# Kernel optimization log

Hardware: AMD Instinct MI355X
Metric: run time of the kernel (lower is better)

The kernel has to match this reference:

```python
import jax, jax.numpy as jnp
import numpy as np

EPS = 1e-6
NEG = -100000.0


def _ln(x):
    # LayerNorm, elementwise_affine=False, eps=1e-6
    mu = jnp.mean(x, axis=-1, keepdims=True)
    var = jnp.mean((x - mu) ** 2, axis=-1, keepdims=True)
    return (x - mu) * jax.lax.rsqrt(var + EPS)


def _split_heads(x, h):
    b, s, d = x.shape
    return x.reshape(b, s, h, d // h).transpose(0, 2, 1, 3)  # [B,H,S,Dh]


def _merge_heads(x):
    b, h, s, dh = x.shape
    return x.transpose(0, 2, 1, 3).reshape(b, s, h * dh)


def _conv_pool(x, w):
    # grouped Conv2d(num_heads -> num_heads, kernel=(4,1), stride=(4,1), groups=num_heads, bias=False)
    # x: [B,H,S,Dh] as NCHW, w: [H,1,4,1] as OIHW
    return jax.lax.conv_general_dilated(
        x, w, window_strides=(4, 1), padding='VALID',
        dimension_numbers=('NCHW', 'OIHW', 'NCHW'),
        feature_group_count=x.shape[1])


def setup_inputs() -> dict:
    key = jax.random.key(0)
    ks = jax.random.split(key, 14)
    B, S, M, D, QKV, MLP, H = 4, 4096, 256, 768, 768, 3072, 12
    std = 0.02
    f = lambda k, shp: jax.random.normal(k, shp, jnp.float32) * std
    return {
        'x': jax.random.normal(ks[0], (B, S, D), jnp.float32),
        'memory': jax.random.normal(ks[1], (B, M, D), jnp.float32),
        'mask': jax.random.randint(ks[2], (B, S), 0, 2).astype(jnp.int32),
        'Wq': f(ks[3], (QKV, D)), 'Wk': f(ks[4], (QKV, D)),
        'Wv': f(ks[5], (QKV, D)), 'Wo': f(ks[6], (D, QKV)),
        'conv_w': f(ks[7], (H, 1, 4, 1)),
        'Uq': f(ks[8], (QKV, D)), 'Uk': f(ks[9], (QKV, D)),
        'Uv': f(ks[10], (QKV, D)), 'Uo': f(ks[11], (D, QKV)),
        'W1': f(ks[12], (MLP, D)), 'W2': f(ks[13], (D, MLP)),
    }


def reference(x, memory, mask, Wq, Wk, Wv, Wo, conv_w, Uq, Uk, Uv, Uo, W1, W2):
    H = conv_w.shape[0]
    maskf = mask.astype(x.dtype)                       # [B,S]

    # ---- pack: ConvAttention(memory as q, x as k/v); conv downsamples k/v ->
    #      shape_change=True so the k_mask is skipped (as in the torch code).
    q = _split_heads(memory @ Wq.T, H)                 # [B,H,M,Dh], unit temperature (log_temp=0)
    k = _split_heads(x @ Wk.T, H)                      # [B,H,S,Dh]
    v = _split_heads(x @ Wv.T, H)
    k = _conv_pool(k, conv_w)                          # [B,H,S//4,Dh]
    v = _conv_pool(v, conv_w)
    logits = jnp.einsum('bhqd,bhkd->bhqk', q, k)
    att = jax.nn.softmax(logits, axis=-1)
    packed = _merge_heads(att @ v) @ Wo.T              # [B,M,D]

    # ---- unpack: TAttention(x as q, packed as k/v) with q_mask injection
    head_dim = Uq.shape[0] // H
    uq = _split_heads(x @ Uq.T, H) * (1.0 / jnp.sqrt(jnp.asarray(head_dim, x.dtype)))
    uk = _split_heads(packed @ Uk.T, H)                # [B,H,M,Dh]
    uv = _split_heads(packed @ Uv.T, H)
    ulogits = jnp.einsum('bhqd,bhkd->bhqk', uq, uk)    # [B,H,S,M]
    ulogits = ulogits + NEG * (1.0 - maskf[:, None, :, None])
    uatt = jax.nn.softmax(ulogits, axis=-1)
    unpacked = _merge_heads(uatt @ uv) @ Uo.T          # [B,S,D]

    unpacked = unpacked * maskf[..., None]
    q_out = _ln(x + unpacked)
    m_out = _ln(memory + packed)

    # FFN: Linear -> GELU(exact) -> Linear (dropout=0)
    h = jax.nn.gelu(jnp.einsum('bsd,md->bsm', q_out, W1), approximate=False)
    y = jnp.einsum('bsm,dm->bsd', h, W2)
    y = y * maskf[..., None]
    q_out = _ln(q_out + y)
    return (q_out, m_out)
```

## Files before the change

kernel.cpp:

```cpp
#include <hip/hip_runtime.h>
#include <hip/hip_bf16.h>
#include <math.h>


typedef unsigned short u16;
typedef __attribute__((ext_vector_type(8))) short bf8v;
typedef __attribute__((ext_vector_type(4))) float f4v;
typedef __attribute__((ext_vector_type(4))) unsigned short us4v;

#define AS1 __attribute__((address_space(1)))
#define AS3 __attribute__((address_space(3)))

__device__ __forceinline__ void gld_lds16(const void* g, void* l) {
  __builtin_amdgcn_global_load_lds((const AS1 unsigned int*)g,
                                   (AS3 unsigned int*)l, 16, 0, 0);
}

__device__ __forceinline__ u16 bf16_rne(float x) {
  unsigned u = __float_as_uint(x);
  return (u16)((u + 0x7fffu + ((u >> 16) & 1u)) >> 16);
}
__device__ __forceinline__ float bf16_to_f(u16 h) {
  return __uint_as_float(((unsigned)h) << 16);
}

struct Cvt8 {
  const float* src[8];
  u16* dst[8];
  int n4[8];
  float sc[8];
  int cum[9];
  int ns;
};
__global__ __launch_bounds__(256) void tobf16_multi_kernel(Cvt8 c) {
  int b = blockIdx.x;
  int seg = 0;
  while (seg + 1 < c.ns && b >= c.cum[seg + 1]) ++seg;
  int i = (b - c.cum[seg]) * 256 + threadIdx.x;
  if (i >= c.n4[seg]) return;
  const float sc = c.sc[seg];
  float4 v = ((const float4*)c.src[seg])[i];
  us4v h;
  h[0] = bf16_rne(v.x * sc); h[1] = bf16_rne(v.y * sc);
  h[2] = bf16_rne(v.z * sc); h[3] = bf16_rne(v.w * sc);
  ((us4v*)c.dst[seg])[i] = h;
}

template <int BM, int BN, int GELU, int OMODE>
__global__ __launch_bounds__(BM * 2) void bgemm_kernel(
    const u16* __restrict__ A, const u16* __restrict__ B,
    float* __restrict__ Cf, u16* __restrict__ Cb, int M, int N, int K,
    int lda, int ldb, int ldc, long long aSB, long long aSH, long long bSB,
    long long bSH, long long cSB, long long cSH, int HB, float scale) {
  constexpr int NJ = BN / 32;
  constexpr int NW = BM / 32;
  constexpr int LPB = (BN / 16) / NW;
  constexpr int VW = 2 + LPB;
  __shared__ u16 smA[3][BM * 32];
  __shared__ u16 smB[3][BN * 32];
  const int t = threadIdx.x;
  const int w = t >> 6, lane = t & 63;
  const int z = blockIdx.z;
  const int bb = z / HB, hh = z % HB;
  const u16* Ab = A + bb * aSB + hh * aSH;
  const u16* Bb = B + bb * bSB + hh * bSH;
  float* Cfb = (OMODE != 1) ? (Cf + bb * cSB + hh * cSH) : nullptr;
  u16* Cbb = (OMODE >= 1) ? (Cb + bb * cSB + hh * cSH) : nullptr;

  const int gx = gridDim.x;
  const int nwg = gx * gridDim.y;
  int f = blockIdx.x + gx * blockIdx.y;
  if ((nwg & 7) == 0) {
    const int cpx = nwg >> 3;
    f = (f & 7) * cpx + (f >> 3);
  }
  const int row0 = (f / gx) * BM, col0 = (f % gx) * BN;

  const int brow_l = lane >> 2;
  const int bchunk = ((lane & 3) ^ ((lane >> 3) & 3)) * 8;
  const int fr = lane & 15;
  const int fq = lane >> 4;
  const int fco = (fq ^ ((lane >> 1) & 3)) * 8;
  const int wr = (w >> 1) * 64, wc = (w & 1) * (BN / 2);

  f4v acc[4][NJ];
#pragma unroll
  for (int i = 0; i < 4; ++i)
#pragma unroll
    for (int j = 0; j < NJ; ++j) acc[i][j] = {0.f, 0.f, 0.f, 0.f};

  const int NT = K >> 5;

  auto stage = [&](int tile, int buf) {
    const int k0 = tile << 5;
#pragma unroll
    for (int i = 0; i < 2; ++i) {
      const int g = w * 2 + i;
      const int r = g * 16 + brow_l;
      gld_lds16(Ab + (long long)(row0 + r) * lda + k0 + bchunk,
                &smA[buf][g * 512 + lane * 8]);
    }
#pragma unroll
    for (int i = 0; i < LPB; ++i) {
      const int g = w * LPB + i;
      const int r = g * 16 + brow_l;
      gld_lds16(Bb + (long long)(col0 + r) * ldb + k0 + bchunk,
                &smB[buf][g * 512 + lane * 8]);
    }
  };
#define WAIT_L()                                            \
  do {                                                      \
    if constexpr (VW == 4)                                  \
      asm volatile("s_waitcnt vmcnt(4)" ::: "memory");      \
    else                                                    \
      asm volatile("s_waitcnt vmcnt(3)" ::: "memory");      \
  } while (0)

  stage(0, 0);
  if (NT > 1) {
    stage(1, 1);
    WAIT_L();
  } else {
    asm volatile("s_waitcnt vmcnt(0)" ::: "memory");
  }
  __builtin_amdgcn_sched_barrier(0);
  __builtin_amdgcn_s_barrier();

  int cur = 0;
  for (int tt = 0; tt < NT; ++tt) {
    const int nn2 = (cur + 2 >= 3) ? cur - 1 : cur + 2;
    if (tt + 2 < NT) stage(tt + 2, nn2);
    {
      bf8v af[4], bfr[NJ];
#pragma unroll
      for (int mi = 0; mi < 4; ++mi)
        af[mi] = *(const bf8v*)&smA[cur][(wr + mi * 16 + fr) * 32 + fco];
#pragma unroll
      for (int nj = 0; nj < NJ; ++nj)
        bfr[nj] = *(const bf8v*)&smB[cur][(wc + nj * 16 + fr) * 32 + fco];
      __builtin_amdgcn_s_setprio(1);
#pragma unroll
      for (int mi = 0; mi < 4; ++mi)
#pragma unroll
        for (int nj = 0; nj < NJ; ++nj)
          acc[mi][nj] = __builtin_amdgcn_mfma_f32_16x16x32_bf16(
              af[mi], bfr[nj], acc[mi][nj], 0, 0, 0);
      __builtin_amdgcn_s_setprio(0);
    }
    if (tt + 2 < NT) {
      WAIT_L();
    } else if (tt + 1 < NT) {
      asm volatile("s_waitcnt vmcnt(0)" ::: "memory");
    }
    __builtin_amdgcn_sched_barrier(0);
    __builtin_amdgcn_s_barrier();
    cur = (cur + 1 >= 3) ? 0 : cur + 1;
  }
#undef WAIT_L

#pragma unroll
  for (int mi = 0; mi < 4; ++mi)
#pragma unroll
    for (int nj = 0; nj < NJ; ++nj) {
      const int col = col0 + wc + nj * 16 + fr;
      const long long base =
          (long long)(row0 + wr + mi * 16 + fq * 4) * ldc + col;
#pragma unroll
      for (int j = 0; j < 4; ++j) {
        float v = acc[mi][nj][j] * scale;
        if (GELU) v = 0.5f * v * (1.f + erff(v * 0.70710678118654752f));
        const long long idx = base + (long long)j * ldc;
        if (OMODE != 1) Cfb[idx] = v;
        if (OMODE >= 1) Cbb[idx] = bf16_rne(v);
      }
    }
}

__global__ __launch_bounds__(512) void fused_pack_attn(
    const u16* __restrict__ q, const u16* __restrict__ k,
    const u16* __restrict__ vt, u16* __restrict__ o) {
  __shared__ char pool[110080];
  u16* smQ = (u16*)pool;
  u16* smK = (u16*)(pool + 16384);
  u16* Pbuf = (u16*)(pool + 32768);
  u16* smV = (u16*)(pool + 98304);
  float* partial = (float*)(pool + 106496);
  float* mold = (float*)(pool + 108544);
  float* fbuf = (float*)(pool + 109056);
  float* srow = (float*)(pool + 109568);

  const int t = threadIdx.x;
  const int w = t >> 6, lane = t & 63;
  const int z = blockIdx.z;
  const int b = z / 12, h = z % 12;
  const int qrow0 = b * 256 + blockIdx.x * 128;
  const long long kvbase = ((long long)(b * 12 + h)) * 65536;

  const int fr = lane & 15, fq = lane >> 4;
  const int fco = (fq ^ ((lane >> 1) & 3)) * 8;
  const int brow_l = lane >> 2;
  const int bchunk = ((lane & 3) ^ ((lane >> 3) & 3)) * 8;
  const int wr = (w >> 2) * 64, wc = (w & 3) * 64;
  const int wrp = (w >> 1) * 32, wcp = (w & 1) * 32;

#pragma unroll
  for (int i = 0; i < 2; ++i) {
    const int g = w * 2 + i;
    const int plane = g >> 3, grp = g & 7;
    gld_lds16(q + (long long)(qrow0 + grp * 16 + brow_l) * 768 + h * 64 +
                  plane * 32 + bchunk,
              smQ + plane * 4096 + grp * 512 + lane * 8);
  }
  if (t < 128) {
    mold[t] = -3.0e38f;
    srow[t] = 0.f;
  }

  f4v acc2[2][2];
#pragma unroll
  for (int i = 0; i < 2; ++i)
#pragma unroll
    for (int j = 0; j < 2; ++j) acc2[i][j] = {0.f, 0.f, 0.f, 0.f};

  for (int kc = 0; kc < 4; ++kc) {
    f4v acc[4][4];
#pragma unroll
    for (int i = 0; i < 4; ++i)
#pragma unroll
      for (int j = 0; j < 4; ++j) acc[i][j] = {0.f, 0.f, 0.f, 0.f};

#pragma unroll
    for (int khalf = 0; khalf < 2; ++khalf) {
      __syncthreads();
#pragma unroll
      for (int i = 0; i < 2; ++i) {
        const int g = w * 2 + i;
        gld_lds16(k + kvbase +
                      (long long)(kc * 256 + g * 16 + brow_l) * 64 +
                      khalf * 32 + bchunk,
                  smK + g * 512 + lane * 8);
      }
      __syncthreads();
#pragma unroll
      for (int mi = 0; mi < 4; ++mi) {
        const bf8v a0 =
            *(const bf8v*)&smQ[khalf * 4096 + (wr + mi * 16 + fr) * 32 + fco];
#pragma unroll
        for (int nj = 0; nj < 4; ++nj) {
          const bf8v b0 = *(const bf8v*)&smK[(wc + nj * 16 + fr) * 32 + fco];
          acc[mi][nj] =
              __builtin_amdgcn_mfma_f32_16x16x32_bf16(a0, b0, acc[mi][nj], 0, 0, 0);
        }
      }
    }
    __syncthreads();

#pragma unroll
    for (int mi = 0; mi < 4; ++mi)
#pragma unroll
      for (int j = 0; j < 4; ++j) {
        float m = fmaxf(fmaxf(acc[mi][0][j], acc[mi][1][j]),
                        fmaxf(acc[mi][2][j], acc[mi][3][j]));
#pragma unroll
        for (int o2 = 1; o2 < 16; o2 <<= 1) m = fmaxf(m, __shfl_xor(m, o2));
        if (fr == 0) partial[(w & 3) * 128 + wr + mi * 16 + fq * 4 + j] = m;
      }
    __syncthreads();
    if (t < 128) {
      const float cm = fmaxf(fmaxf(partial[t], partial[128 + t]),
                             fmaxf(partial[256 + t], partial[384 + t]));
      const float mnew = fmaxf(mold[t], cm);
      fbuf[t] = exp2f(mold[t] - mnew);
      mold[t] = mnew;
    }
    __syncthreads();

#pragma unroll
    for (int mi = 0; mi < 4; ++mi)
#pragma unroll
      for (int j = 0; j < 4; ++j) {
        const int row = wr + mi * 16 + fq * 4 + j;
        const float rm = mold[row];
        float s = 0.f;
#pragma unroll
        for (int nj = 0; nj < 4; ++nj) {
          const float e = exp2f(acc[mi][nj][j] - rm);
          s += e;
          const int col = wc + nj * 16 + fr;
          const int kc2 = col >> 5, kloc = col & 31;
          Pbuf[kc2 * 4096 + row * 32 + (((kloc >> 3) ^ ((row >> 1) & 3)) * 8) +
               (kloc & 7)] = bf16_rne(e);
        }
#pragma unroll
        for (int o2 = 1; o2 < 16; o2 <<= 1) s += __shfl_xor(s, o2);
        if (fr == 0) partial[(w & 3) * 128 + row] = s;
      }
    if (w < 4) {
      gld_lds16(vt + kvbase + (long long)(w * 16 + brow_l) * 1024 + kc * 256 +
                    bchunk,
                smV + w * 512 + lane * 8);
    }
    __syncthreads();
    if (t < 128)
      srow[t] = srow[t] * fbuf[t] +
                ((partial[t] + partial[128 + t]) +
                 (partial[256 + t] + partial[384 + t]));
    __syncthreads();

#pragma unroll
    for (int mi = 0; mi < 2; ++mi)
#pragma unroll
      for (int j = 0; j < 4; ++j) {
        const float fr_ = fbuf[wrp + mi * 16 + fq * 4 + j];
        acc2[mi][0][j] *= fr_;
        acc2[mi][1][j] *= fr_;
      }

    for (int sk = 0; sk < 8; ++sk) {
      const int cur = (sk & 1) * 2048;
      if (sk < 7 && w < 4) {
        gld_lds16(vt + kvbase + (long long)(w * 16 + brow_l) * 1024 +
                      kc * 256 + (sk + 1) * 32 + bchunk,
                  smV + (2048 - cur) + w * 512 + lane * 8);
      }
#pragma unroll
      for (int mi = 0; mi < 2; ++mi) {
        const bf8v pa =
            *(const bf8v*)&Pbuf[sk * 4096 + (wrp + mi * 16 + fr) * 32 + fco];
#pragma unroll
        for (int nj = 0; nj < 2; ++nj) {
          const bf8v v0 =
              *(const bf8v*)&smV[cur + (wcp + nj * 16 + fr) * 32 + fco];
          acc2[mi][nj] =
              __builtin_amdgcn_mfma_f32_16x16x32_bf16(pa, v0, acc2[mi][nj], 0, 0, 0);
        }
      }
      __syncthreads();
    }
  }

  if (t < 128) fbuf[t] = 1.f / srow[t];
  __syncthreads();
  const long long ooff = (long long)qrow0 * 768 + h * 64;
#pragma unroll
  for (int mi = 0; mi < 2; ++mi)
#pragma unroll
    for (int nj = 0; nj < 2; ++nj)
#pragma unroll
      for (int j = 0; j < 4; ++j) {
        const int row = wrp + mi * 16 + fq * 4 + j;
        const int col = wcp + nj * 16 + fr;
        o[ooff + (long long)row * 768 + col] =
            bf16_rne(acc2[mi][nj][j] * fbuf[row]);
      }
}

__global__ __launch_bounds__(512) void fused_unpack_attn(
    const u16* __restrict__ q, int ldq, const u16* __restrict__ k, int ldk,
    const u16* __restrict__ vt, u16* __restrict__ o) {
  __shared__ char pool[76800];
  u16* smA = (u16*)pool;
  u16* smB = (u16*)(pool + 8192);
  u16* Pbuf = (u16*)pool;
  u16* smV = (u16*)(pool + 65536);
  float* partial = (float*)(pool + 73728);
  float* rowmax = (float*)(pool + 75776);
  float* rowsum = (float*)(pool + 76288);

  const int t = threadIdx.x;
  const int w = t >> 6, lane = t & 63;
  const int z = blockIdx.z;
  const int b = z / 12, h = z % 12;
  const int q0 = blockIdx.x * 128;

  const long long qoff = (long long)(b * 4096 + q0) * ldq + h * 64;
  const long long koff = (long long)(b * 256) * ldk + h * 64;
  const long long vbase = ((long long)(b * 12 + h)) * 16384;
  const long long ooff = (long long)(b * 4096 + q0) * 768 + h * 64;

  const int fr = lane & 15, fq = lane >> 4;
  const int fco = (fq ^ ((lane >> 1) & 3)) * 8;
  const int brow_l = lane >> 2;
  const int bchunk = ((lane & 3) ^ ((lane >> 3) & 3)) * 8;

  const int wr = (w >> 2) * 64, wc = (w & 3) * 64;
  f4v acc[4][4];
#pragma unroll
  for (int i = 0; i < 4; ++i)
#pragma unroll
    for (int j = 0; j < 4; ++j) acc[i][j] = {0.f, 0.f, 0.f, 0.f};

  for (int k0 = 0; k0 < 64; k0 += 32) {
    __syncthreads();
#pragma unroll
    for (int i = 0; i < 2; ++i) {
      const int g = w * 2 + i;
      const int r = g * 16 + brow_l;
      gld_lds16(k + koff + (long long)r * ldk + k0 + bchunk,
                smB + g * 512 + lane * 8);
    }
    {
      const int r = w * 16 + brow_l;
      gld_lds16(q + qoff + (long long)r * ldq + k0 + bchunk,
                smA + w * 512 + lane * 8);
    }
    __syncthreads();
#pragma unroll
    for (int mi = 0; mi < 4; ++mi) {
      const bf8v a0 = *(const bf8v*)&smA[(wr + mi * 16 + fr) * 32 + fco];
#pragma unroll
      for (int nj = 0; nj < 4; ++nj) {
        const bf8v b0 = *(const bf8v*)&smB[(wc + nj * 16 + fr) * 32 + fco];
        acc[mi][nj] = __builtin_amdgcn_mfma_f32_16x16x32_bf16(a0, b0, acc[mi][nj], 0, 0, 0);
      }
    }
  }
  __syncthreads();

  if (w < 4) {
    const int r = w * 16 + brow_l;
    gld_lds16(vt + vbase + (long long)r * 256 + bchunk,
              smV + w * 512 + lane * 8);
  }

#pragma unroll
  for (int mi = 0; mi < 4; ++mi)
#pragma unroll
    for (int j = 0; j < 4; ++j) {
      float m = fmaxf(fmaxf(acc[mi][0][j], acc[mi][1][j]),
                      fmaxf(acc[mi][2][j], acc[mi][3][j]));
#pragma unroll
      for (int o2 = 1; o2 < 16; o2 <<= 1) m = fmaxf(m, __shfl_xor(m, o2));
      if (fr == 0) partial[(w & 3) * 128 + wr + mi * 16 + fq * 4 + j] = m;
    }
  __syncthreads();
  if (t < 128)
    rowmax[t] = fmaxf(fmaxf(partial[t], partial[128 + t]),
                      fmaxf(partial[256 + t], partial[384 + t]));
  __syncthreads();
#pragma unroll
  for (int mi = 0; mi < 4; ++mi)
#pragma unroll
    for (int j = 0; j < 4; ++j) {
      const int row = wr + mi * 16 + fq * 4 + j;
      const float rm = rowmax[row];
      float s = 0.f;
#pragma unroll
      for (int nj = 0; nj < 4; ++nj) {
        const float e = exp2f(acc[mi][nj][j] - rm);
        s += e;
        const int col = wc + nj * 16 + fr;
        const int kc = col >> 5, kloc = col & 31;
        Pbuf[kc * 4096 + row * 32 + (((kloc >> 3) ^ ((row >> 1) & 3)) * 8) +
             (kloc & 7)] = bf16_rne(e);
      }
#pragma unroll
      for (int o2 = 1; o2 < 16; o2 <<= 1) s += __shfl_xor(s, o2);
      if (fr == 0) partial[(w & 3) * 128 + row] = s;
    }
  __syncthreads();
  if (t < 128)
    rowsum[t] = 1.f / ((partial[t] + partial[128 + t]) +
                       (partial[256 + t] + partial[384 + t]));
  __syncthreads();

  const int wrp = (w >> 1) * 32, wcp = (w & 1) * 32;
  f4v acc2[2][2];
#pragma unroll
  for (int i = 0; i < 2; ++i)
#pragma unroll
    for (int j = 0; j < 2; ++j) acc2[i][j] = {0.f, 0.f, 0.f, 0.f};

  for (int kc = 0; kc < 8; ++kc) {
    const int cur = (kc & 1) * 2048;
    if (kc < 7 && w < 4) {
      const int r = w * 16 + brow_l;
      gld_lds16(vt + vbase + (long long)r * 256 + (kc + 1) * 32 + bchunk,
                smV + (2048 - cur) + w * 512 + lane * 8);
    }
#pragma unroll
    for (int mi = 0; mi < 2; ++mi) {
      const bf8v pa =
          *(const bf8v*)&Pbuf[kc * 4096 + (wrp + mi * 16 + fr) * 32 + fco];
#pragma unroll
      for (int nj = 0; nj < 2; ++nj) {
        const bf8v v0 =
            *(const bf8v*)&smV[cur + (wcp + nj * 16 + fr) * 32 + fco];
        acc2[mi][nj] = __builtin_amdgcn_mfma_f32_16x16x32_bf16(pa, v0, acc2[mi][nj], 0, 0, 0);
      }
    }
    __syncthreads();
  }
#pragma unroll
  for (int mi = 0; mi < 2; ++mi)
#pragma unroll
    for (int nj = 0; nj < 2; ++nj)
#pragma unroll
      for (int j = 0; j < 4; ++j) {
        const int row = wrp + mi * 16 + fq * 4 + j;
        const int col = wcp + nj * 16 + fr;
        o[ooff + (long long)row * 768 + col] =
            bf16_rne(acc2[mi][nj][j] * rowsum[row]);
      }
}

__global__ __launch_bounds__(256) void conv_dual_kernel(
    const u16* __restrict__ in, const float* __restrict__ w,
    u16* __restrict__ ok, u16* __restrict__ ovT, int total, int ld) {
  int idx = blockIdx.x * 256 + threadIdx.x;
  if (idx >= total) return;
  const int dh = idx & 63;
  int r = idx >> 6;
  const int tt = r & 1023; r >>= 10;
  const int h = r % 12;
  const int b = r / 12;
  const long long s = ((long long)(b * 4096 + 4 * tt)) * ld + h * 64 + dh;
  const float* wh = w + h * 4;
  float vk = 0.f, vv = 0.f;
#pragma unroll
  for (int j = 0; j < 4; ++j) {
    vk = fmaf(wh[j], bf16_to_f(in[s + j * ld]), vk);
    vv = fmaf(wh[j], bf16_to_f(in[s + 768 + j * ld]), vv);
  }
  ok[idx] = bf16_rne(vk);
  ovT[(((long long)(b * 12 + h)) * 64 + dh) * 1024 + tt] = bf16_rne(vv);
}

__global__ __launch_bounds__(256) void transT_b2b_kernel(
    const u16* __restrict__ in, u16* __restrict__ o, int total, int ld) {
  int idx = blockIdx.x * 256 + threadIdx.x;
  if (idx >= total) return;
  const int key = idx & 255;
  int r = idx >> 8;
  const int dh = r & 63; r >>= 6;
  const int h = r % 12;
  const int b = r / 12;
  o[idx] = in[((long long)(b * 256 + key)) * ld + h * 64 + dh];
}

template <int BBF16>
__global__ __launch_bounds__(256) void ln_kernel(
    const float* __restrict__ a, const float* __restrict__ bf,
    const u16* __restrict__ bb, const int* __restrict__ mask,
    float* __restrict__ out, u16* __restrict__ outb) {
  const long long row = blockIdx.x;
  const float* pa = a + row * 768;
  const float ms = mask ? (float)mask[row] : 1.f;
  __shared__ float buf[768];
  __shared__ float red[4];
  const int t = threadIdx.x;
  float lsum = 0.f;
#pragma unroll
  for (int i = t; i < 768; i += 256) {
    const float bvv = BBF16 ? bf16_to_f(bb[row * 768 + i]) : bf[row * 768 + i];
    const float v = fmaf(bvv, ms, pa[i]);
    buf[i] = v;
    lsum += v;
  }
  for (int o = 32; o; o >>= 1) lsum += __shfl_xor(lsum, o);
  if ((t & 63) == 0) red[t >> 6] = lsum;
  __syncthreads();
  const float mu = (red[0] + red[1] + red[2] + red[3]) * (1.f / 768.f);
  float lvar = 0.f;
#pragma unroll
  for (int i = t; i < 768; i += 256) {
    const float d = buf[i] - mu;
    lvar = fmaf(d, d, lvar);
  }
  __syncthreads();
  for (int o = 32; o; o >>= 1) lvar += __shfl_xor(lvar, o);
  if ((t & 63) == 0) red[t >> 6] = lvar;
  __syncthreads();
  const float var = (red[0] + red[1] + red[2] + red[3]) * (1.f / 768.f);
  const float rstd = rsqrtf(var + 1e-6f);
  float* po = out + row * 768;
  u16* pob = outb ? outb + row * 768 : nullptr;
#pragma unroll
  for (int i = t; i < 768; i += 256) {
    const float v = (buf[i] - mu) * rstd;
    po[i] = v;
    if (outb) pob[i] = bf16_rne(v);
  }
}

extern "C" void kernel_launch(void* const* d_in, const int* in_sizes, int n_in,
                              void* d_out, int out_size, void* d_ws,
                              size_t ws_size, hipStream_t stream) {
  const float* x = (const float*)d_in[0];
  const float* memory = (const float*)d_in[1];
  const int* mask = (const int*)d_in[2];
  const float* Wq = (const float*)d_in[3];
  const float* Wk = (const float*)d_in[4];
  const float* Wv = (const float*)d_in[5];
  const float* Wo = (const float*)d_in[6];
  const float* conv_w = (const float*)d_in[7];
  const float* Uq = (const float*)d_in[8];
  const float* Uk = (const float*)d_in[9];
  const float* Uv = (const float*)d_in[10];
  const float* Uo = (const float*)d_in[11];
  const float* W1 = (const float*)d_in[12];
  const float* W2 = (const float*)d_in[13];
  float* out = (float*)d_out;
  float* ws = (float*)d_ws;

  const int XR = 16384, MR = 1024, D = 768, MLP = 3072;
  const long long CB = 3145728;
  const int WD = 589824;
  const int WM = 2359296;

  float* A0 = ws + 0;
  float* A1 = ws + 18874368;
  float* A2 = ws + 31457280;

  u16* xb    = (u16*)(A0 + 12582912);
  u16* kvqb  = (u16*)A0;
  u16* uattvb = (u16*)A1;
  u16* unpb  = (u16*)A0;
  float* qout1 = A0 + 6291456;
  u16* qout1b = (u16*)(out + 6291456);
  u16* hb    = (u16*)A1;
  float* ybuf = A2;

  u16* kpb  = (u16*)A2;
  u16* vpTb = kpb + 3145728;
  u16* qpb  = (u16*)(A2 + 3145728);
  u16* memb = qpb + 786432;
  u16* avmb = (u16*)(A2 + 3932160);
  u16* pkb  = avmb + 786432;
  float* packed = A2 + 4718592;
  u16* ukvb = (u16*)(A2 + 5505024);
  u16* uvTb = (u16*)(A2 + 6291456);
  u16* wp16 = (u16*)(A2 + 7077888);

  u16* Wkvqb = wp16;
  u16* Wqb = wp16 + 2304 * 768;
  u16* Wob = Wqb + WD;
  u16* Ukvb2 = wp16;
  u16* Uob = wp16 + 1536 * 768;
  u16* W1b = wp16;
  u16* W2b = wp16 + WM;

  const float UQS = 0.18033688011112042592f;
  const float L2E = 1.4426950408889634074f;

  {
    Cvt8 c{};
    const float* ss[7] = {x, memory, Wk, Wv, Uq, Wq, Wo};
    u16* dd[7] = {xb, memb, Wkvqb, Wkvqb + WD, Wkvqb + 2 * WD, Wqb, Wob};
    int nn[7] = {3145728, 196608, WD / 4, WD / 4, WD / 4, WD / 4, WD / 4};
    float sc[7] = {1.f, 1.f, 1.f, 1.f, UQS, 1.f, 1.f};
    int cum = 0;
    for (int i = 0; i < 7; ++i) {
      c.src[i] = ss[i]; c.dst[i] = dd[i]; c.n4[i] = nn[i]; c.sc[i] = sc[i];
      c.cum[i] = cum; cum += (nn[i] + 255) / 256;
    }
    c.cum[7] = cum; c.ns = 7;
    tobf16_multi_kernel<<<cum, 256, 0, stream>>>(c);
  }
  bgemm_kernel<256, 128, 0, 1><<<dim3(18, 64, 1), 512, 0, stream>>>(
      xb, Wkvqb, nullptr, kvqb, XR, 2304, D, D, D, 2304,
      0, 0, 0, 0, 0, 0, 1, 1.f);
  bgemm_kernel<128, 128, 0, 1><<<dim3(6, 8, 1), 256, 0, stream>>>(
      memb, Wqb, nullptr, qpb, MR, D, D, D, D, D, 0, 0, 0, 0, 0, 0, 1, L2E);
  conv_dual_kernel<<<12288, 256, 0, stream>>>(kvqb, conv_w, kpb, vpTb,
                                              3145728, 2304);
  {
    dim3 g(2, 1, 48);
    fused_pack_attn<<<g, 512, 0, stream>>>(qpb, kpb, vpTb, avmb);
  }
  bgemm_kernel<128, 128, 0, 2><<<dim3(6, 8, 1), 256, 0, stream>>>(
      avmb, Wob, packed, pkb, MR, D, D, D, D, D, 0, 0, 0, 0, 0, 0, 1, 1.f);
  ln_kernel<0><<<MR, 256, 0, stream>>>(memory, packed, nullptr, nullptr,
                                       out + 12582912, nullptr);

  {
    Cvt8 c{};
    const float* ss[3] = {Uk, Uv, Uo};
    u16* dd[3] = {Ukvb2, Ukvb2 + WD, Uob};
    int cum = 0;
    for (int i = 0; i < 3; ++i) {
      c.src[i] = ss[i]; c.dst[i] = dd[i]; c.n4[i] = WD / 4; c.sc[i] = 1.f;
      c.cum[i] = cum; cum += (WD / 4 + 255) / 256;
    }
    c.cum[3] = cum; c.ns = 3;
    tobf16_multi_kernel<<<cum, 256, 0, stream>>>(c);
  }
  bgemm_kernel<128, 128, 0, 1><<<dim3(12, 8, 1), 256, 0, stream>>>(
      pkb, Ukvb2, nullptr, ukvb, MR, 1536, D, D, D, 1536,
      0, 0, 0, 0, 0, 0, 1, 1.f);
  transT_b2b_kernel<<<3072, 256, 0, stream>>>(ukvb + 768, uvTb, 786432, 1536);
  {
    dim3 g(32, 1, 48);
    fused_unpack_attn<<<g, 512, 0, stream>>>(kvqb + 1536, 2304, ukvb, 1536,
                                             uvTb, uattvb);
  }
  bgemm_kernel<256, 128, 0, 1><<<dim3(6, 16, 4), 512, 0, stream>>>(
      uattvb, Uob, nullptr, unpb, 4096, D, D, D, D, D,
      CB, 0, 0, 0, CB, 0, 1, 1.f);
  ln_kernel<1><<<XR, 256, 0, stream>>>(x, nullptr, unpb, mask, qout1, qout1b);

  {
    Cvt8 c{};
    const float* ss[2] = {W1, W2};
    u16* dd[2] = {W1b, W2b};
    int cum = 0;
    for (int i = 0; i < 2; ++i) {
      c.src[i] = ss[i]; c.dst[i] = dd[i]; c.n4[i] = WM / 4; c.sc[i] = 1.f;
      c.cum[i] = cum; cum += (WM / 4 + 255) / 256;
    }
    c.cum[2] = cum; c.ns = 2;
    tobf16_multi_kernel<<<cum, 256, 0, stream>>>(c);
  }
  for (int c = 0; c < 2; ++c) {
    bgemm_kernel<256, 128, 1, 1><<<dim3(24, 16, 2), 512, 0, stream>>>(
        qout1b + (long long)c * 2 * CB, W1b, nullptr, hb, 4096, MLP, D,
        D, D, MLP, CB, 0, 0, 0, 12582912, 0, 1, 1.f);
    bgemm_kernel<128, 128, 0, 0><<<dim3(6, 32, 2), 256, 0, stream>>>(
        hb, W2b, ybuf, nullptr, 4096, D, MLP, MLP, MLP, D,
        12582912, 0, 0, 0, CB, 0, 1, 1.f);
    ln_kernel<0><<<8192, 256, 0, stream>>>(qout1 + (long long)c * 2 * CB, ybuf,
                                           nullptr, mask + c * 8192,
                                           out + (long long)c * 2 * CB, nullptr);
  }
}
```

Measured before the change: 638.9 us.

## Fix GEMM tile at 128x128 and deepen LDS pipeline to four stages

Removes the BM/BN template parameters so every bf16 GEMM uses 128x128 tiles with 256 threads, and moves the global-to-LDS prefetch from a 3-buffer/2-ahead ring to a 4-buffer/3-ahead ring with matching vmcnt waits. The large GEMMs that used 256x128 tiles with 512 threads now launch twice as many smaller blocks. The aim is to hide more load latency and possibly raise occupancy, in exchange for more LDS per block (64KB) and less operand reuse per tile. The prologue now stages three tiles unconditionally, which assumes K has at least three 32-wide tiles.

```diff
diff --git a/kernel.cpp b/kernel.cpp
--- a/kernel.cpp
+++ b/kernel.cpp
@@ -46,18 +46,14 @@
   ((us4v*)c.dst[seg])[i] = h;
 }
 
-template <int BM, int BN, int GELU, int OMODE>
-__global__ __launch_bounds__(BM * 2) void bgemm_kernel(
+template <int GELU, int OMODE>
+__global__ __launch_bounds__(256) void bgemm_kernel(
     const u16* __restrict__ A, const u16* __restrict__ B,
     float* __restrict__ Cf, u16* __restrict__ Cb, int M, int N, int K,
     int lda, int ldb, int ldc, long long aSB, long long aSH, long long bSB,
     long long bSH, long long cSB, long long cSH, int HB, float scale) {
-  constexpr int NJ = BN / 32;
-  constexpr int NW = BM / 32;
-  constexpr int LPB = (BN / 16) / NW;
-  constexpr int VW = 2 + LPB;
-  __shared__ u16 smA[3][BM * 32];
-  __shared__ u16 smB[3][BN * 32];
+  __shared__ u16 smA[4][4096];
+  __shared__ u16 smB[4][4096];
   const int t = threadIdx.x;
   const int w = t >> 6, lane = t & 63;
   const int z = blockIdx.z;
@@ -74,20 +70,20 @@
     const int cpx = nwg >> 3;
     f = (f & 7) * cpx + (f >> 3);
   }
-  const int row0 = (f / gx) * BM, col0 = (f % gx) * BN;
+  const int row0 = (f / gx) * 128, col0 = (f % gx) * 128;
 
   const int brow_l = lane >> 2;
   const int bchunk = ((lane & 3) ^ ((lane >> 3) & 3)) * 8;
   const int fr = lane & 15;
   const int fq = lane >> 4;
   const int fco = (fq ^ ((lane >> 1) & 3)) * 8;
-  const int wr = (w >> 1) * 64, wc = (w & 1) * (BN / 2);
-
-  f4v acc[4][NJ];
+  const int wr = (w >> 1) * 64, wc = (w & 1) * 64;
+
+  f4v acc[4][4];
 #pragma unroll
   for (int i = 0; i < 4; ++i)
 #pragma unroll
-    for (int j = 0; j < NJ; ++j) acc[i][j] = {0.f, 0.f, 0.f, 0.f};
+    for (int j = 0; j < 4; ++j) acc[i][j] = {0.f, 0.f, 0.f, 0.f};
 
   const int NT = K >> 5;
 
@@ -101,67 +97,56 @@
                 &smA[buf][g * 512 + lane * 8]);
     }
 #pragma unroll
-    for (int i = 0; i < LPB; ++i) {
-      const int g = w * LPB + i;
+    for (int i = 0; i < 2; ++i) {
+      const int g = w * 2 + i;
       const int r = g * 16 + brow_l;
       gld_lds16(Bb + (long long)(col0 + r) * ldb + k0 + bchunk,
                 &smB[buf][g * 512 + lane * 8]);
     }
   };
-#define WAIT_L()                                            \
-  do {                                                      \
-    if constexpr (VW == 4)                                  \
-      asm volatile("s_waitcnt vmcnt(4)" ::: "memory");      \
-    else                                                    \
-      asm volatile("s_waitcnt vmcnt(3)" ::: "memory");      \
-  } while (0)
 
   stage(0, 0);
-  if (NT > 1) {
-    stage(1, 1);
-    WAIT_L();
-  } else {
-    asm volatile("s_waitcnt vmcnt(0)" ::: "memory");
-  }
+  stage(1, 1);
+  stage(2, 2);
+  asm volatile("s_waitcnt vmcnt(8)" ::: "memory");
   __builtin_amdgcn_sched_barrier(0);
   __builtin_amdgcn_s_barrier();
 
-  int cur = 0;
   for (int tt = 0; tt < NT; ++tt) {
-    const int nn2 = (cur + 2 >= 3) ? cur - 1 : cur + 2;
-    if (tt + 2 < NT) stage(tt + 2, nn2);
+    const int cur = tt & 3;
+    if (tt + 3 < NT) stage(tt + 3, (tt + 3) & 3);
     {
-      bf8v af[4], bfr[NJ];
+      bf8v af[4], bfr[4];
 #pragma unroll
       for (int mi = 0; mi < 4; ++mi)
         af[mi] = *(const bf8v*)&smA[cur][(wr + mi * 16 + fr) * 32 + fco];
 #pragma unroll
-      for (int nj = 0; nj < NJ; ++nj)
+      for (int nj = 0; nj < 4; ++nj)
         bfr[nj] = *(const bf8v*)&smB[cur][(wc + nj * 16 + fr) * 32 + fco];
       __builtin_amdgcn_s_setprio(1);
 #pragma unroll
       for (int mi = 0; mi < 4; ++mi)
 #pragma unroll
-        for (int nj = 0; nj < NJ; ++nj)
+        for (int nj = 0; nj < 4; ++nj)
           acc[mi][nj] = __builtin_amdgcn_mfma_f32_16x16x32_bf16(
               af[mi], bfr[nj], acc[mi][nj], 0, 0, 0);
       __builtin_amdgcn_s_setprio(0);
     }
-    if (tt + 2 < NT) {
-      WAIT_L();
+    if (tt + 3 < NT) {
+      asm volatile("s_waitcnt vmcnt(8)" ::: "memory");
+    } else if (tt + 2 < NT) {
+      asm volatile("s_waitcnt vmcnt(4)" ::: "memory");
     } else if (tt + 1 < NT) {
       asm volatile("s_waitcnt vmcnt(0)" ::: "memory");
     }
     __builtin_amdgcn_sched_barrier(0);
     __builtin_amdgcn_s_barrier();
-    cur = (cur + 1 >= 3) ? 0 : cur + 1;
-  }
-#undef WAIT_L
+  }
 
 #pragma unroll
   for (int mi = 0; mi < 4; ++mi)
 #pragma unroll
-    for (int nj = 0; nj < NJ; ++nj) {
+    for (int nj = 0; nj < 4; ++nj) {
       const int col = col0 + wc + nj * 16 + fr;
       const long long base =
           (long long)(row0 + wr + mi * 16 + fq * 4) * ldc + col;
@@ -657,10 +642,10 @@
     c.cum[7] = cum; c.ns = 7;
     tobf16_multi_kernel<<<cum, 256, 0, stream>>>(c);
   }
-  bgemm_kernel<256, 128, 0, 1><<<dim3(18, 64, 1), 512, 0, stream>>>(
+  bgemm_kernel<0, 1><<<dim3(18, 128, 1), 256, 0, stream>>>(
       xb, Wkvqb, nullptr, kvqb, XR, 2304, D, D, D, 2304,
       0, 0, 0, 0, 0, 0, 1, 1.f);
-  bgemm_kernel<128, 128, 0, 1><<<dim3(6, 8, 1), 256, 0, stream>>>(
+  bgemm_kernel<0, 1><<<dim3(6, 8, 1), 256, 0, stream>>>(
       memb, Wqb, nullptr, qpb, MR, D, D, D, D, D, 0, 0, 0, 0, 0, 0, 1, L2E);
   conv_dual_kernel<<<12288, 256, 0, stream>>>(kvqb, conv_w, kpb, vpTb,
                                               3145728, 2304);
@@ -668,7 +653,7 @@
     dim3 g(2, 1, 48);
     fused_pack_attn<<<g, 512, 0, stream>>>(qpb, kpb, vpTb, avmb);
   }
-  bgemm_kernel<128, 128, 0, 2><<<dim3(6, 8, 1), 256, 0, stream>>>(
+  bgemm_kernel<0, 2><<<dim3(6, 8, 1), 256, 0, stream>>>(
       avmb, Wob, packed, pkb, MR, D, D, D, D, D, 0, 0, 0, 0, 0, 0, 1, 1.f);
   ln_kernel<0><<<MR, 256, 0, stream>>>(memory, packed, nullptr, nullptr,
                                        out + 12582912, nullptr);
@@ -685,7 +670,7 @@
     c.cum[3] = cum; c.ns = 3;
     tobf16_multi_kernel<<<cum, 256, 0, stream>>>(c);
   }
-  bgemm_kernel<128, 128, 0, 1><<<dim3(12, 8, 1), 256, 0, stream>>>(
+  bgemm_kernel<0, 1><<<dim3(12, 8, 1), 256, 0, stream>>>(
       pkb, Ukvb2, nullptr, ukvb, MR, 1536, D, D, D, 1536,
       0, 0, 0, 0, 0, 0, 1, 1.f);
   transT_b2b_kernel<<<3072, 256, 0, stream>>>(ukvb + 768, uvTb, 786432, 1536);
@@ -694,7 +679,7 @@
     fused_unpack_attn<<<g, 512, 0, stream>>>(kvqb + 1536, 2304, ukvb, 1536,
                                              uvTb, uattvb);
   }
-  bgemm_kernel<256, 128, 0, 1><<<dim3(6, 16, 4), 512, 0, stream>>>(
+  bgemm_kernel<0, 1><<<dim3(6, 32, 4), 256, 0, stream>>>(
       uattvb, Uob, nullptr, unpb, 4096, D, D, D, D, D,
       CB, 0, 0, 0, CB, 0, 1, 1.f);
   ln_kernel<1><<<XR, 256, 0, stream>>>(x, nullptr, unpb, mask, qout1, qout1b);
@@ -712,10 +697,10 @@
     tobf16_multi_kernel<<<cum, 256, 0, stream>>>(c);
   }
   for (int c = 0; c < 2; ++c) {
-    bgemm_kernel<256, 128, 1, 1><<<dim3(24, 16, 2), 512, 0, stream>>>(
+    bgemm_kernel<1, 1><<<dim3(24, 32, 2), 256, 0, stream>>>(
         qout1b + (long long)c * 2 * CB, W1b, nullptr, hb, 4096, MLP, D,
         D, D, MLP, CB, 0, 0, 0, 12582912, 0, 1, 1.f);
-    bgemm_kernel<128, 128, 0, 0><<<dim3(6, 32, 2), 256, 0, stream>>>(
+    bgemm_kernel<0, 0><<<dim3(6, 32, 2), 256, 0, stream>>>(
         hb, W2b, ybuf, nullptr, 4096, D, MLP, MLP, MLP, D,
         12582912, 0, 0, 0, CB, 0, 1, 1.f);
     ln_kernel<0><<<8192, 256, 0, stream>>>(qout1 + (long long)c * 2 * CB, ybuf,
```

New measurement: 690.3 us. +8.1%, slower.
